# Kernel tuning notes

Measured on AMD Instinct MI355X. Metric: run time of the kernel, lower is better.

The kernel has to match this reference:

```python
import jax, jax.numpy as jnp
import numpy as np

N, D_IN, D_K = 8192, 512, 64


def setup_inputs() -> dict:
    key = jax.random.key(0)
    k0, k1, k2, k3 = jax.random.split(key, 4)
    return {
        "inputs": jax.random.normal(k0, (N, D_IN), dtype=jnp.float32),
        "Wq": jax.random.normal(k1, (D_K, D_IN), dtype=jnp.float32),
        "Wk": jax.random.normal(k2, (D_K, D_IN), dtype=jnp.float32),
        "Wv": jax.random.normal(k3, (D_K, D_IN), dtype=jnp.float32),
    }


def reference(inputs, Wq, Wk, Wv):
    # nn.Linear(bias=False): x @ W.T, W has shape [out, in]
    q = inputs @ Wq.T  # [N, Dk]
    k = inputs @ Wk.T  # [N, Dk]
    v = inputs @ Wv.T  # [N, Dk]
    scaled = (q @ k.T) / jnp.sqrt(jnp.float32(D_K))  # [N, N]
    attn = jax.nn.softmax(scaled, axis=1)            # softmax over keys (dim=1)
    # weighted = values[:,None] * attn.T[:,:,None]; sum over dim 0 == attn @ v
    return attn @ v  # [N, Dk]
```

## Files before the change

### kernel.cpp

```cpp
#include <hip/hip_runtime.h>
#include <hip/hip_bf16.h>


#define N_TOK 8192
#define D_INN 512
#define DK    64

typedef __attribute__((ext_vector_type(8))) short bf16x8;
typedef __attribute__((ext_vector_type(4))) float f32x4;

static __device__ __forceinline__ unsigned f2bf_u(float f) {
  union { float f; unsigned u; } v; v.f = f;
  return (v.u + 0x7FFFu + ((v.u >> 16) & 1u)) >> 16;
}
static __device__ __forceinline__ unsigned short f2bf(float f) { return (unsigned short)f2bf_u(f); }
static __device__ __forceinline__ float bf2f(unsigned short h) {
  union { unsigned u; float f; } v; v.u = ((unsigned)h) << 16; return v.f;
}
static __device__ __forceinline__ unsigned truncpk(float a, float b) {
  union { float f; unsigned u; } x, y; x.f = a; y.f = b;
  return (x.u >> 16) | (y.u & 0xFFFF0000u);
}
static __device__ __forceinline__ void split2(float a, float b, unsigned& hi, unsigned& lo) {
  unsigned ha = f2bf_u(a), hb = f2bf_u(b);
  float ra = a - bf2f((unsigned short)ha);
  float rb = b - bf2f((unsigned short)hb);
  hi = ha | (hb << 16);
  lo = f2bf_u(ra) | (f2bf_u(rb) << 16);
}

__global__ __launch_bounds__(256) void split_x(const float* __restrict__ X,
                                               unsigned* __restrict__ xh,
                                               unsigned* __restrict__ xl) {
  int i = blockIdx.x * 256 + threadIdx.x;
  const float4 a = *(const float4*)(X + i * 8);
  const float4 b = *(const float4*)(X + i * 8 + 4);
  uint4 H, L;
  split2(a.x, a.y, H.x, L.x);
  split2(a.z, a.w, H.y, L.y);
  split2(b.x, b.y, H.z, L.z);
  split2(b.z, b.w, H.w, L.w);
  *(uint4*)(xh + i * 4) = H;
  *(uint4*)(xl + i * 4) = L;
}

__global__ __launch_bounds__(256) void prep_w(
    const float* __restrict__ Wq, const float* __restrict__ Wk, const float* __restrict__ Wv,
    unsigned short* __restrict__ wh, unsigned short* __restrict__ wl) {
  int t = blockIdx.x * 256 + threadIdx.x;
  if (t >= 192 * 512) return;
  const float* src = (t < 64 * 512) ? Wq : ((t < 128 * 512) ? Wk : Wv);
  float x = src[t & (64 * 512 - 1)];
  unsigned short h = f2bf(x);
  wh[t] = h;
  wl[t] = f2bf(x - bf2f(h));
}

__global__ __launch_bounds__(256, 2) void qkv2(
    const unsigned short* __restrict__ xh, const unsigned short* __restrict__ xl,
    const unsigned short* __restrict__ wh, const unsigned short* __restrict__ wl,
    unsigned short* __restrict__ qhp, unsigned short* __restrict__ qlp,
    unsigned short* __restrict__ kph, unsigned short* __restrict__ kpl,
    unsigned short* __restrict__ vp) {
  const int tid = threadIdx.x, w = tid >> 6, l = tid & 63;
  const int l15 = l & 15, g = l >> 4;
  const int t0 = blockIdx.x * 16;
  const int dq = w * 16;

  f32x4 aq = {0.f, 0.f, 0.f, 0.f}, ak = aq, av = aq;

  for (int kc = 0; kc < D_INN; kc += 32) {
    const int xoff = (t0 + l15) * D_INN + kc + g * 8;
    bf16x8 ah = *(const bf16x8*)(xh + xoff);
    bf16x8 al = *(const bf16x8*)(xl + xoff);
    const int wq_off = (dq + l15) * D_INN + kc + g * 8;
    const int wk_off = (64 + dq + l15) * D_INN + kc + g * 8;
    const int wv_off = (128 + dq + l15) * D_INN + kc + g * 8;
    bf16x8 bqh = *(const bf16x8*)(wh + wq_off);
    bf16x8 bql = *(const bf16x8*)(wl + wq_off);
    bf16x8 bkh = *(const bf16x8*)(wh + wk_off);
    bf16x8 bkl = *(const bf16x8*)(wl + wk_off);
    bf16x8 bvh = *(const bf16x8*)(wh + wv_off);
    aq = __builtin_amdgcn_mfma_f32_16x16x32_bf16(ah, bqh, aq, 0, 0, 0);
    aq = __builtin_amdgcn_mfma_f32_16x16x32_bf16(ah, bql, aq, 0, 0, 0);
    aq = __builtin_amdgcn_mfma_f32_16x16x32_bf16(al, bqh, aq, 0, 0, 0);
    ak = __builtin_amdgcn_mfma_f32_16x16x32_bf16(ah, bkh, ak, 0, 0, 0);
    ak = __builtin_amdgcn_mfma_f32_16x16x32_bf16(ah, bkl, ak, 0, 0, 0);
    ak = __builtin_amdgcn_mfma_f32_16x16x32_bf16(al, bkh, ak, 0, 0, 0);
    av = __builtin_amdgcn_mfma_f32_16x16x32_bf16(ah, bvh, av, 0, 0, 0);
    av = __builtin_amdgcn_mfma_f32_16x16x32_bf16(al, bvh, av, 0, 0, 0);
  }

#pragma unroll
  for (int r = 0; r < 4; r++) {
    float v = aq[r] * 0.125f;
    int row = t0 + g * 4 + r;
    unsigned short h = f2bf(v);
    qhp[row * DK + dq + l15] = h;
    qlp[row * DK + dq + l15] = f2bf(v - bf2f(h));
  }
#pragma unroll
  for (int r = 0; r < 4; r++) {
    float v = ak[r];
    int t = t0 + g * 4 + r;
    int d = dq + l15;
    int off = (t >> 5) * 2048 + ((t >> 4) & 1) * 1024 + (d >> 5) * 512 +
              ((t & 15) + (((d >> 3) & 3) << 4)) * 8 + (d & 7);
    unsigned short h = f2bf(v);
    kph[off] = h;
    kpl[off] = f2bf(v - bf2f(h));
  }
  {
    int tg = t0 + g * 4;
    int d = dq + l15;
    int off = (tg >> 5) * 2048 + (d >> 4) * 512 +
              (((d & 15) + (((tg >> 3) & 3) << 4))) * 8 + (tg & 7);
    uint2 pk;
    pk.x = f2bf_u(av[0]) | (f2bf_u(av[1]) << 16);
    pk.y = f2bf_u(av[2]) | (f2bf_u(av[3]) << 16);
    *(uint2*)(vp + off) = pk;
  }
}

__global__ __launch_bounds__(256, 2) void attn3(
    const unsigned short* __restrict__ qhp, const unsigned short* __restrict__ qlp,
    const unsigned short* __restrict__ kph, const unsigned short* __restrict__ kpl,
    const unsigned short* __restrict__ vp,
    float* __restrict__ pnum, float* __restrict__ pden, float* __restrict__ pM) {
  __shared__ unsigned short P_lds[4 * 2 * 16 * 72];

  const int tid = threadIdx.x, w = tid >> 6, l = tid & 63;
  const int l15 = l & 15, g = l >> 4;
  const int qblk = blockIdx.x >> 3, ks = blockIdx.x & 7;
  const int wq0 = qblk * 128 + w * 32;

  bf16x8 qhf[2][2], qlf[2][2];
#pragma unroll
  for (int u = 0; u < 2; u++)
#pragma unroll
    for (int c = 0; c < 2; c++) {
      int row = wq0 + u * 16 + l15;
      qhf[u][c] = *(const bf16x8*)(qhp + row * DK + c * 32 + g * 8);
      qlf[u][c] = *(const bf16x8*)(qlp + row * DK + c * 32 + g * 8);
    }

  const short onec = (short)0x3F80;
  const bf16x8 ones = {onec, onec, onec, onec, onec, onec, onec, onec};

  f32x4 accO[2][4], accL[2];
  float m[2] = {-1e30f, -1e30f};
#pragma unroll
  for (int u = 0; u < 2; u++) {
    accL[u] = f32x4{0.f, 0.f, 0.f, 0.f};
#pragma unroll
    for (int ds = 0; ds < 4; ds++) accO[u][ds] = f32x4{0.f, 0.f, 0.f, 0.f};
  }

  for (int kt = ks * 1024; kt < ks * 1024 + 1024; kt += 64) {
    const int kti = kt >> 5;

    f32x4 st[2][4];
#pragma unroll
    for (int s = 0; s < 4; s++) {
      bf16x8 khf[2], klf[2];
#pragma unroll
      for (int c = 0; c < 2; c++) {
        const int off = (kti + (s >> 1)) * 2048 + (s & 1) * 1024 + c * 512 + l * 8;
        khf[c] = *(const bf16x8*)(kph + off);
        klf[c] = *(const bf16x8*)(kpl + off);
      }
      __builtin_amdgcn_s_setprio(1);
#pragma unroll
      for (int u = 0; u < 2; u++) {
        f32x4 sa = {0.f, 0.f, 0.f, 0.f};
        sa = __builtin_amdgcn_mfma_f32_16x16x32_bf16(khf[0], qhf[u][0], sa, 0, 0, 0);
        sa = __builtin_amdgcn_mfma_f32_16x16x32_bf16(khf[1], qhf[u][1], sa, 0, 0, 0);
        sa = __builtin_amdgcn_mfma_f32_16x16x32_bf16(khf[0], qlf[u][0], sa, 0, 0, 0);
        sa = __builtin_amdgcn_mfma_f32_16x16x32_bf16(khf[1], qlf[u][1], sa, 0, 0, 0);
        sa = __builtin_amdgcn_mfma_f32_16x16x32_bf16(klf[0], qhf[u][0], sa, 0, 0, 0);
        sa = __builtin_amdgcn_mfma_f32_16x16x32_bf16(klf[1], qhf[u][1], sa, 0, 0, 0);
        st[u][s] = sa;
      }
      __builtin_amdgcn_s_setprio(0);
    }

    bf16x8 vb[4][2];
#pragma unroll
    for (int ds = 0; ds < 4; ds++)
#pragma unroll
      for (int c = 0; c < 2; c++)
        vb[ds][c] = *(const bf16x8*)(vp + (kti + c) * 2048 + ds * 512 + l * 8);

    bf16x8 pa[2][2];
#pragma unroll
    for (int u = 0; u < 2; u++) {
      float t0m = fmaxf(fmaxf(st[u][0][0], st[u][0][1]), fmaxf(st[u][0][2], st[u][0][3]));
      float t1m = fmaxf(fmaxf(st[u][1][0], st[u][1][1]), fmaxf(st[u][1][2], st[u][1][3]));
      float t2m = fmaxf(fmaxf(st[u][2][0], st[u][2][1]), fmaxf(st[u][2][2], st[u][2][3]));
      float t3m = fmaxf(fmaxf(st[u][3][0], st[u][3][1]), fmaxf(st[u][3][2], st[u][3][3]));
      float tm = fmaxf(fmaxf(t0m, t1m), fmaxf(t2m, t3m));
      tm = fmaxf(tm, __shfl_xor(tm, 16, 64));
      tm = fmaxf(tm, __shfl_xor(tm, 32, 64));
      if (__any(tm > m[u] + 8.f)) {
        float mn = fmaxf(m[u], tm);
        float fac = __expf(m[u] - mn);
        m[u] = mn;
#pragma unroll
        for (int r = 0; r < 4; r++) {
          float fr = __shfl(fac, g * 4 + r, 64);
          accL[u][r] *= fr;
#pragma unroll
          for (int ds = 0; ds < 4; ds++) accO[u][ds][r] *= fr;
        }
      }
      const int base = ((w * 2 + u) * 16 + l15) * 72;
#pragma unroll
      for (int s = 0; s < 4; s++) {
        float p0 = __expf(st[u][s][0] - m[u]);
        float p1 = __expf(st[u][s][1] - m[u]);
        float p2 = __expf(st[u][s][2] - m[u]);
        float p3 = __expf(st[u][s][3] - m[u]);
        *(unsigned*)&P_lds[base + s * 16 + g * 4]     = truncpk(p0, p1);
        *(unsigned*)&P_lds[base + s * 16 + g * 4 + 2] = truncpk(p2, p3);
      }
#pragma unroll
      for (int c = 0; c < 2; c++)
        pa[u][c] = *(const bf16x8*)&P_lds[base + c * 32 + g * 8];
      accL[u] = __builtin_amdgcn_mfma_f32_16x16x32_bf16(pa[u][0], ones, accL[u], 0, 0, 0);
      accL[u] = __builtin_amdgcn_mfma_f32_16x16x32_bf16(pa[u][1], ones, accL[u], 0, 0, 0);
    }

    __builtin_amdgcn_s_setprio(1);
#pragma unroll
    for (int ds = 0; ds < 4; ds++)
#pragma unroll
      for (int u = 0; u < 2; u++) {
        accO[u][ds] = __builtin_amdgcn_mfma_f32_16x16x32_bf16(pa[u][0], vb[ds][0], accO[u][ds], 0, 0, 0);
        accO[u][ds] = __builtin_amdgcn_mfma_f32_16x16x32_bf16(pa[u][1], vb[ds][1], accO[u][ds], 0, 0, 0);
      }
    __builtin_amdgcn_s_setprio(0);
  }

#pragma unroll
  for (int u = 0; u < 2; u++) {
#pragma unroll
    for (int ds = 0; ds < 4; ds++)
#pragma unroll
      for (int r = 0; r < 4; r++)
        pnum[(size_t)ks * (N_TOK * DK) + (wq0 + u * 16 + g * 4 + r) * DK + ds * 16 + l15] =
            accO[u][ds][r];
    if (l15 == 0) {
#pragma unroll
      for (int r = 0; r < 4; r++) pden[ks * N_TOK + wq0 + u * 16 + g * 4 + r] = accL[u][r];
    }
    if (g == 0) pM[ks * N_TOK + wq0 + u * 16 + l15] = m[u];
  }
}

__global__ __launch_bounds__(256) void merge8(
    const float* __restrict__ pnum, const float* __restrict__ pden,
    const float* __restrict__ pM, float* __restrict__ out) {
  int i = blockIdx.x * 256 + threadIdx.x;
  int q = i >> 6, d = i & 63;
  float M = -1e30f;
#pragma unroll
  for (int s = 0; s < 8; s++) M = fmaxf(M, pM[s * N_TOK + q]);
  float num = 0.f, den = 0.f;
#pragma unroll
  for (int s = 0; s < 8; s++) {
    float e = __expf(pM[s * N_TOK + q] - M);
    num += pnum[(size_t)s * (N_TOK * DK) + q * DK + d] * e;
    den += pden[s * N_TOK + q] * e;
  }
  out[i] = num / den;
}

extern "C" void kernel_launch(void* const* d_in, const int* in_sizes, int n_in,
                              void* d_out, int out_size, void* d_ws, size_t ws_size,
                              hipStream_t stream) {
  (void)in_sizes; (void)n_in; (void)out_size; (void)ws_size;
  const float* X  = (const float*)d_in[0];
  const float* Wq = (const float*)d_in[1];
  const float* Wk = (const float*)d_in[2];
  const float* Wv = (const float*)d_in[3];

  char* base = (char*)d_ws;
  unsigned short* xh  = (unsigned short*)(base);
  unsigned short* xl  = (unsigned short*)(base + 8388608);
  unsigned short* qhp = (unsigned short*)(base + 16777216);
  unsigned short* qlp = (unsigned short*)(base + 17825792);
  unsigned short* kph = (unsigned short*)(base + 18874368);
  unsigned short* kpl = (unsigned short*)(base + 19922944);
  unsigned short* vp  = (unsigned short*)(base + 20971520);
  unsigned short* wh  = (unsigned short*)(base + 22020096);
  unsigned short* wl  = (unsigned short*)(base + 22216704);
  float* pden = (float*)(base + 22020096);
  float* pM   = (float*)(base + 22282240);
  float* pnum = (float*)(base);

  split_x<<<(N_TOK * D_INN) / (256 * 8), 256, 0, stream>>>(X, (unsigned*)xh, (unsigned*)xl);
  prep_w<<<384, 256, 0, stream>>>(Wq, Wk, Wv, wh, wl);
  qkv2<<<N_TOK / 16, 256, 0, stream>>>(xh, xl, wh, wl, qhp, qlp, kph, kpl, vp);
  attn3<<<512, 256, 0, stream>>>(qhp, qlp, kph, kpl, vp, pnum, pden, pM);
  merge8<<<(N_TOK * DK) / 256, 256, 0, stream>>>(pnum, pden, pM, (float*)d_out);
}
```

Baseline: 153.5 us.

## Fuse input split into QKV kernel, double key splits, store partials in bf16

Removes the separate split_x pass: the QKV projection kernel now reads fp32 inputs directly and splits them into hi/lo bf16 in registers, which avoids writing and re-reading the bf16 copies. The attention kernel now uses 16 key splits instead of 8 with a higher occupancy hint, giving 1024 blocks for better CU fill. Partial numerators are stored as bf16 to halve merge traffic, at some cost in accuracy. The workspace layout is adjusted to fit the larger pden/pM arrays.

```diff
diff --git a/kernel.cpp b/kernel.cpp
--- a/kernel.cpp
+++ b/kernel.cpp
@@ -27,21 +27,6 @@
   float rb = b - bf2f((unsigned short)hb);
   hi = ha | (hb << 16);
   lo = f2bf_u(ra) | (f2bf_u(rb) << 16);
-}
-
-__global__ __launch_bounds__(256) void split_x(const float* __restrict__ X,
-                                               unsigned* __restrict__ xh,
-                                               unsigned* __restrict__ xl) {
-  int i = blockIdx.x * 256 + threadIdx.x;
-  const float4 a = *(const float4*)(X + i * 8);
-  const float4 b = *(const float4*)(X + i * 8 + 4);
-  uint4 H, L;
-  split2(a.x, a.y, H.x, L.x);
-  split2(a.z, a.w, H.y, L.y);
-  split2(b.x, b.y, H.z, L.z);
-  split2(b.z, b.w, H.w, L.w);
-  *(uint4*)(xh + i * 4) = H;
-  *(uint4*)(xl + i * 4) = L;
 }
 
 __global__ __launch_bounds__(256) void prep_w(
@@ -56,8 +41,8 @@
   wl[t] = f2bf(x - bf2f(h));
 }
 
-__global__ __launch_bounds__(256, 2) void qkv2(
-    const unsigned short* __restrict__ xh, const unsigned short* __restrict__ xl,
+__global__ __launch_bounds__(256, 2) void qkv3(
+    const float* __restrict__ X,
     const unsigned short* __restrict__ wh, const unsigned short* __restrict__ wl,
     unsigned short* __restrict__ qhp, unsigned short* __restrict__ qlp,
     unsigned short* __restrict__ kph, unsigned short* __restrict__ kpl,
@@ -70,9 +55,16 @@
   f32x4 aq = {0.f, 0.f, 0.f, 0.f}, ak = aq, av = aq;
 
   for (int kc = 0; kc < D_INN; kc += 32) {
-    const int xoff = (t0 + l15) * D_INN + kc + g * 8;
-    bf16x8 ah = *(const bf16x8*)(xh + xoff);
-    bf16x8 al = *(const bf16x8*)(xl + xoff);
+    const float* xp = X + (t0 + l15) * D_INN + kc + g * 8;
+    float4 x0 = *(const float4*)xp;
+    float4 x1 = *(const float4*)(xp + 4);
+    union { unsigned u[4]; bf16x8 v; } ahu, alu;
+    split2(x0.x, x0.y, ahu.u[0], alu.u[0]);
+    split2(x0.z, x0.w, ahu.u[1], alu.u[1]);
+    split2(x1.x, x1.y, ahu.u[2], alu.u[2]);
+    split2(x1.z, x1.w, ahu.u[3], alu.u[3]);
+    bf16x8 ah = ahu.v, al = alu.v;
+
     const int wq_off = (dq + l15) * D_INN + kc + g * 8;
     const int wk_off = (64 + dq + l15) * D_INN + kc + g * 8;
     const int wv_off = (128 + dq + l15) * D_INN + kc + g * 8;
@@ -122,16 +114,16 @@
   }
 }
 
-__global__ __launch_bounds__(256, 2) void attn3(
+__global__ __launch_bounds__(256, 4) void attn4(
     const unsigned short* __restrict__ qhp, const unsigned short* __restrict__ qlp,
     const unsigned short* __restrict__ kph, const unsigned short* __restrict__ kpl,
     const unsigned short* __restrict__ vp,
-    float* __restrict__ pnum, float* __restrict__ pden, float* __restrict__ pM) {
+    unsigned short* __restrict__ pnb, float* __restrict__ pden, float* __restrict__ pM) {
   __shared__ unsigned short P_lds[4 * 2 * 16 * 72];
 
   const int tid = threadIdx.x, w = tid >> 6, l = tid & 63;
   const int l15 = l & 15, g = l >> 4;
-  const int qblk = blockIdx.x >> 3, ks = blockIdx.x & 7;
+  const int qblk = blockIdx.x >> 4, ks = blockIdx.x & 15;
   const int wq0 = qblk * 128 + w * 32;
 
   bf16x8 qhf[2][2], qlf[2][2];
@@ -156,7 +148,7 @@
     for (int ds = 0; ds < 4; ds++) accO[u][ds] = f32x4{0.f, 0.f, 0.f, 0.f};
   }
 
-  for (int kt = ks * 1024; kt < ks * 1024 + 1024; kt += 64) {
+  for (int kt = ks * 512; kt < ks * 512 + 512; kt += 64) {
     const int kti = kt >> 5;
 
     f32x4 st[2][4];
@@ -247,8 +239,8 @@
     for (int ds = 0; ds < 4; ds++)
 #pragma unroll
       for (int r = 0; r < 4; r++)
-        pnum[(size_t)ks * (N_TOK * DK) + (wq0 + u * 16 + g * 4 + r) * DK + ds * 16 + l15] =
-            accO[u][ds][r];
+        pnb[(size_t)ks * (N_TOK * DK) + (wq0 + u * 16 + g * 4 + r) * DK + ds * 16 + l15] =
+            f2bf(accO[u][ds][r]);
     if (l15 == 0) {
 #pragma unroll
       for (int r = 0; r < 4; r++) pden[ks * N_TOK + wq0 + u * 16 + g * 4 + r] = accL[u][r];
@@ -257,19 +249,19 @@
   }
 }
 
-__global__ __launch_bounds__(256) void merge8(
-    const float* __restrict__ pnum, const float* __restrict__ pden,
+__global__ __launch_bounds__(256) void merge16(
+    const unsigned short* __restrict__ pnb, const float* __restrict__ pden,
     const float* __restrict__ pM, float* __restrict__ out) {
   int i = blockIdx.x * 256 + threadIdx.x;
   int q = i >> 6, d = i & 63;
   float M = -1e30f;
 #pragma unroll
-  for (int s = 0; s < 8; s++) M = fmaxf(M, pM[s * N_TOK + q]);
+  for (int s = 0; s < 16; s++) M = fmaxf(M, pM[s * N_TOK + q]);
   float num = 0.f, den = 0.f;
 #pragma unroll
-  for (int s = 0; s < 8; s++) {
+  for (int s = 0; s < 16; s++) {
     float e = __expf(pM[s * N_TOK + q] - M);
-    num += pnum[(size_t)s * (N_TOK * DK) + q * DK + d] * e;
+    num += bf2f(pnb[(size_t)s * (N_TOK * DK) + q * DK + d]) * e;
     den += pden[s * N_TOK + q] * e;
   }
   out[i] = num / den;
@@ -285,8 +277,7 @@
   const float* Wv = (const float*)d_in[3];
 
   char* base = (char*)d_ws;
-  unsigned short* xh  = (unsigned short*)(base);
-  unsigned short* xl  = (unsigned short*)(base + 8388608);
+  unsigned short* pnb = (unsigned short*)(base);
   unsigned short* qhp = (unsigned short*)(base + 16777216);
   unsigned short* qlp = (unsigned short*)(base + 17825792);
   unsigned short* kph = (unsigned short*)(base + 18874368);
@@ -295,12 +286,10 @@
   unsigned short* wh  = (unsigned short*)(base + 22020096);
   unsigned short* wl  = (unsigned short*)(base + 22216704);
   float* pden = (float*)(base + 22020096);
-  float* pM   = (float*)(base + 22282240);
-  float* pnum = (float*)(base);
-
-  split_x<<<(N_TOK * D_INN) / (256 * 8), 256, 0, stream>>>(X, (unsigned*)xh, (unsigned*)xl);
+  float* pM   = (float*)(base + 22544384);
+
   prep_w<<<384, 256, 0, stream>>>(Wq, Wk, Wv, wh, wl);
-  qkv2<<<N_TOK / 16, 256, 0, stream>>>(xh, xl, wh, wl, qhp, qlp, kph, kpl, vp);
-  attn3<<<512, 256, 0, stream>>>(qhp, qlp, kph, kpl, vp, pnum, pden, pM);
-  merge8<<<(N_TOK * DK) / 256, 256, 0, stream>>>(pnum, pden, pM, (float*)d_out);
-}
+  qkv3<<<N_TOK / 16, 256, 0, stream>>>(X, wh, wl, qhp, qlp, kph, kpl, vp);
+  attn4<<<1024, 256, 0, stream>>>(qhp, qlp, kph, kpl, vp, pnb, pden, pM);
+  merge16<<<(N_TOK * DK) / 256, 256, 0, stream>>>(pnb, pden, pM, (float*)d_out);
+}
```

New measurement: 205.5 us. 33.9% more time.
